# Optimization experiments

Measured on AMD Instinct MI355X. Metric: run time of the kernel, lower is better.

Reference implementation:

```python
import jax, jax.numpy as jnp
import numpy as np

N_NODES = 100000
N_EDGES = 1200000
NODE_DIM = 128
HIDDEN = 64
N_POSTS = 50000


def setup_inputs() -> dict:
    key = jax.random.key(0)
    ks = jax.random.split(key, 10)
    s = 1.0 / np.sqrt(NODE_DIM)
    sh = 1.0 / np.sqrt(HIDDEN)
    return {
        "node_features": jax.random.normal(ks[0], (N_NODES, NODE_DIM), dtype=jnp.float32),
        "edge_index": jax.random.randint(ks[1], (2, N_EDGES), 0, N_NODES, dtype=jnp.int64) if jax.config.jax_enable_x64 else jax.random.randint(ks[1], (2, N_EDGES), 0, N_NODES, dtype=jnp.int32),
        "post_mask": jax.random.randint(ks[2], (N_POSTS,), 0, N_NODES, dtype=jnp.int32),
        "W_enc": jax.random.uniform(ks[3], (NODE_DIM, HIDDEN), jnp.float32, -s, s),
        "b_enc": jax.random.uniform(ks[4], (HIDDEN,), jnp.float32, -s, s),
        "W_conv": jax.random.uniform(ks[5], (HIDDEN, HIDDEN), jnp.float32, -sh, sh),
        "b_conv": jax.random.uniform(ks[6], (HIDDEN,), jnp.float32, -sh, sh),
        "W_out": jax.random.uniform(ks[7], (HIDDEN, 1), jnp.float32, -sh, sh),
        "b_out": jax.random.uniform(ks[8], (1,), jnp.float32, -sh, sh),
    }


def reference(node_features, edge_index, post_mask, W_enc, b_enc, W_conv, b_conv, W_out, b_out):
    # encode: relu(Linear)
    node_emb = jax.nn.relu(node_features @ W_enc + b_enc)  # [N, H]
    src, dst = edge_index[0], edge_index[1]
    # per-edge gather then scatter-add into destination nodes (segment sum)
    messages = jax.ops.segment_sum(node_emb[src], dst, num_segments=node_emb.shape[0])  # [N, H]
    node_emb = jax.nn.relu((node_emb + messages) @ W_conv + b_conv)  # [N, H]
    post_emb = node_emb[post_mask]  # [P, H]
    out = jax.nn.sigmoid((post_emb @ W_out + b_out).squeeze(-1))  # [P]
    return out
```

## Files before the change

kernel.cpp:

```cpp
#include <hip/hip_runtime.h>
#include <hip/hip_bf16.h>
#include <math.h>


#define HIDDEN 64
#define NODE_DIM 128
#define SCAN_CHUNK 1024

typedef __attribute__((ext_vector_type(8))) short short8;
typedef __attribute__((ext_vector_type(4))) float floatx4;

union F2B { short8 s; __hip_bfloat162 h[4]; };

__device__ inline short8 cvt8(const float4& p, const float4& q) {
    F2B u;
    u.h[0] = __float22bfloat162_rn(make_float2(p.x, p.y));
    u.h[1] = __float22bfloat162_rn(make_float2(p.z, p.w));
    u.h[2] = __float22bfloat162_rn(make_float2(q.x, q.y));
    u.h[3] = __float22bfloat162_rn(make_float2(q.z, q.w));
    return u.s;
}

__device__ inline void cvt8_split(const float4& p, const float4& q,
                                  short8& hi, short8& lo) {
    const float f[8] = {p.x, p.y, p.z, p.w, q.x, q.y, q.z, q.w};
    F2B uh, ul;
    #pragma unroll
    for (int jj = 0; jj < 4; ++jj) {
        const float2 v = make_float2(f[2 * jj], f[2 * jj + 1]);
        const __hip_bfloat162 h = __float22bfloat162_rn(v);
        const float2 hv = __bfloat1622float2(h);
        ul.h[jj] = __float22bfloat162_rn(make_float2(v.x - hv.x, v.y - hv.y));
        uh.h[jj] = h;
    }
    hi = uh.s; lo = ul.s;
}

__global__ __launch_bounds__(256) void k_pre(
    const int* __restrict__ post, unsigned int* __restrict__ bits,
    int* __restrict__ nodelist, int* __restrict__ listCnt,
    int* __restrict__ count, int n_posts, int n_nodes)
{
    const int gtid = blockIdx.x * 256 + threadIdx.x;
    if (gtid < n_nodes) count[gtid] = 0;
    if (gtid < n_posts) {
        const int n = post[gtid];
        const unsigned int bit = 1u << (n & 31);
        const unsigned int old = atomicOr(&bits[n >> 5], bit);
        if (!(old & bit)) {
            const int i = atomicAdd(listCnt, 1);
            nodelist[i] = n;
        }
    }
}

__global__ __launch_bounds__(256) void k_encode_count(
    const float* __restrict__ A, const float* __restrict__ We,
    const float* __restrict__ be, __hip_bfloat16* __restrict__ emb16,
    const int* __restrict__ dsts, const unsigned int* __restrict__ bits,
    int* __restrict__ count, int n_nodes, int n_tiles, int n_edges)
{
    const int lane = threadIdx.x & 63;
    const int r    = lane & 15;
    const int quad = lane >> 4;

    short8 Wb[4][4];
    #pragma unroll
    for (int ks = 0; ks < 4; ++ks)
        #pragma unroll
        for (int nt = 0; nt < 4; ++nt) {
            F2B u;
            #pragma unroll
            for (int jj = 0; jj < 4; ++jj) {
                const int k0 = ks * 32 + quad * 8 + 2 * jj;
                const float lo = We[(size_t)k0 * HIDDEN + nt * 16 + r];
                const float hi = We[(size_t)(k0 + 1) * HIDDEN + nt * 16 + r];
                u.h[jj] = __float22bfloat162_rn(make_float2(lo, hi));
            }
            Wb[ks][nt] = u.s;
        }
    float bias[4];
    #pragma unroll
    for (int nt = 0; nt < 4; ++nt) bias[nt] = be[nt * 16 + r];

    const int wid    = (blockIdx.x * 256 + threadIdx.x) >> 6;
    const int nwaves = gridDim.x * 4;
    for (int t = wid; t < n_tiles; t += nwaves) {
        const float* Arow = A + (size_t)t * 16 * NODE_DIM + (size_t)r * NODE_DIM + quad * 8;
        float4 a[4][2];
        #pragma unroll
        for (int ks = 0; ks < 4; ++ks) {
            a[ks][0] = *(const float4*)(Arow + ks * 32);
            a[ks][1] = *(const float4*)(Arow + ks * 32 + 4);
        }
        floatx4 acc[4] = {};
        #pragma unroll
        for (int ks = 0; ks < 4; ++ks) {
            const short8 af = cvt8(a[ks][0], a[ks][1]);
            #pragma unroll
            for (int nt = 0; nt < 4; ++nt)
                acc[nt] = __builtin_amdgcn_mfma_f32_16x16x32_bf16(af, Wb[ks][nt], acc[nt], 0, 0, 0);
        }
        #pragma unroll
        for (int nt = 0; nt < 4; ++nt)
            #pragma unroll
            for (int g = 0; g < 4; ++g) {
                const int node = t * 16 + quad * 4 + g;
                const float h = fmaxf(acc[nt][g] + bias[nt], 0.0f);
                emb16[(size_t)node * HIDDEN + nt * 16 + r] = __float2bfloat16(h);
            }
    }
    const int rem = n_nodes - n_tiles * 16;
    if (rem > 0 && wid == 0) {
        for (int n = n_tiles * 16; n < n_nodes; ++n) {
            float acc = be[lane];
            const float* row = A + (size_t)n * NODE_DIM;
            for (int k = 0; k < NODE_DIM; ++k)
                acc = fmaf(row[k], We[(size_t)k * HIDDEN + lane], acc);
            emb16[(size_t)n * HIDDEN + lane] = __float2bfloat16(fmaxf(acc, 0.0f));
        }
    }

    const int stride = gridDim.x * 256;
    for (int e = blockIdx.x * 256 + threadIdx.x; e < n_edges; e += stride) {
        const int d = dsts[e];
        if ((bits[d >> 5] >> (d & 31)) & 1u) atomicAdd(&count[d], 1);
    }
}

__global__ __launch_bounds__(256) void k_scan_lb(
    const int* __restrict__ count, int* __restrict__ row_start,
    unsigned int* __restrict__ partials, int n)
{
    __shared__ int s[256];
    __shared__ int sExc;
    const int b = blockIdx.x, tid = threadIdx.x;
    const int base = b * SCAN_CHUNK + tid * 4;
    int c0 = (base + 0 < n) ? count[base + 0] : 0;
    int c1 = (base + 1 < n) ? count[base + 1] : 0;
    int c2 = (base + 2 < n) ? count[base + 2] : 0;
    int c3 = (base + 3 < n) ? count[base + 3] : 0;
    const int t = c0 + c1 + c2 + c3;
    s[tid] = t;
    __syncthreads();
    #pragma unroll
    for (int off = 1; off < 256; off <<= 1) {
        int v = (tid >= off) ? s[tid - off] : 0;
        __syncthreads();
        s[tid] += v;
        __syncthreads();
    }
    const int total = s[255];

    if (b == 0) {
        if (tid == 0) {
            __hip_atomic_store(&partials[0], (2u << 30) | (unsigned int)total,
                               __ATOMIC_RELEASE, __HIP_MEMORY_SCOPE_AGENT);
            sExc = 0;
        }
    } else {
        if (tid == 0) {
            __hip_atomic_store(&partials[b], (1u << 30) | (unsigned int)total,
                               __ATOMIC_RELEASE, __HIP_MEMORY_SCOPE_AGENT);
        }
        if (tid < 64) {
            int exc = 0;
            int winEnd = b;
            while (true) {
                const int j = winEnd - 64 + tid;
                const unsigned int v = (j >= 0)
                    ? __hip_atomic_load(&partials[j], __ATOMIC_ACQUIRE,
                                        __HIP_MEMORY_SCOPE_AGENT)
                    : (2u << 30);
                const unsigned int st = v >> 30;
                if (__ballot(st == 0u)) {
                    __builtin_amdgcn_s_sleep(1);
                    continue;
                }
                const unsigned long long b2 = __ballot(st == 2u);
                int contrib;
                bool done;
                if (b2) {
                    const int hi = 63 - __clzll(b2);
                    contrib = (tid >= hi) ? (int)(v & 0x3FFFFFFFu) : 0;
                    done = true;
                } else {
                    contrib = (int)(v & 0x3FFFFFFFu);
                    done = false;
                }
                #pragma unroll
                for (int off = 1; off < 64; off <<= 1)
                    contrib += __shfl_xor(contrib, off);
                exc += contrib;
                if (done) break;
                winEnd -= 64;
            }
            if (tid == 0) {
                __hip_atomic_store(&partials[b],
                                   (2u << 30) | (unsigned int)(exc + total),
                                   __ATOMIC_RELEASE, __HIP_MEMORY_SCOPE_AGENT);
                sExc = exc;
            }
        }
    }
    __syncthreads();
    int run = sExc + s[tid] - t;
    if (base + 0 < n) row_start[base + 0] = run;           run += c0;
    if (base + 1 < n) row_start[base + 1] = run;           run += c1;
    if (base + 2 < n) row_start[base + 2] = run;           run += c2;
    if (base + 3 < n) row_start[base + 3] = run;
}

__global__ __launch_bounds__(256) void k_fill(
    const int* __restrict__ srcs, const int* __restrict__ dsts,
    const unsigned int* __restrict__ bits, int* __restrict__ row_start,
    int* __restrict__ slots, int n_edges)
{
    const int stride = gridDim.x * 256;
    for (int e = blockIdx.x * 256 + threadIdx.x; e < n_edges; e += stride) {
        const int d = dsts[e];
        if (!((bits[d >> 5] >> (d & 31)) & 1u)) continue;
        const int idx = atomicAdd(&row_start[d], 1);
        slots[idx] = srcs[e];
    }
}

__global__ __launch_bounds__(256) void k_gather(
    const int* __restrict__ nodelist, const int* __restrict__ listCnt,
    const int* __restrict__ row_end, const int* __restrict__ count,
    const int* __restrict__ slots, const __hip_bfloat16* __restrict__ emb16,
    float* __restrict__ msg_c)
{
    const int lane = threadIdx.x & 63;
    const int j    = lane & 7;
    const int g    = lane >> 3;
    const int gw   = (blockIdx.x * 256 + threadIdx.x) >> 6;
    const int nw   = gridDim.x * 4;
    const int nc   = listCnt[0];

    for (int i = gw; i < nc; i += nw) {
        const int n    = nodelist[i];
        const int m    = count[n];
        const int base = row_end[n] - m;

        float2 a0 = {0.f, 0.f}, a1 = {0.f, 0.f}, a2 = {0.f, 0.f}, a3 = {0.f, 0.f};
        #define ACC8(v)  do { F2B u; u.s = (v); float2 t;                       \
            t = __bfloat1622float2(u.h[0]); a0.x += t.x; a0.y += t.y;           \
            t = __bfloat1622float2(u.h[1]); a1.x += t.x; a1.y += t.y;           \
            t = __bfloat1622float2(u.h[2]); a2.x += t.x; a2.y += t.y;           \
            t = __bfloat1622float2(u.h[3]); a3.x += t.x; a3.y += t.y; } while (0)

        if (g == 0) {
            const short8 v = *(const short8*)(emb16 + (size_t)n * HIDDEN + j * 8);
            ACC8(v);
        }
        int c = g;
        for (; c + 8 < m; c += 16) {
            const int s0 = slots[base + c];
            const int s1 = slots[base + c + 8];
            const short8 v0 = *(const short8*)(emb16 + (size_t)s0 * HIDDEN + j * 8);
            const short8 v1 = *(const short8*)(emb16 + (size_t)s1 * HIDDEN + j * 8);
            ACC8(v0); ACC8(v1);
        }
        for (; c < m; c += 8) {
            const int s0 = slots[base + c];
            const short8 v0 = *(const short8*)(emb16 + (size_t)s0 * HIDDEN + j * 8);
            ACC8(v0);
        }
        #undef ACC8

        #pragma unroll
        for (int off = 8; off < 64; off <<= 1) {
            a0.x += __shfl_xor(a0.x, off); a0.y += __shfl_xor(a0.y, off);
            a1.x += __shfl_xor(a1.x, off); a1.y += __shfl_xor(a1.y, off);
            a2.x += __shfl_xor(a2.x, off); a2.y += __shfl_xor(a2.y, off);
            a3.x += __shfl_xor(a3.x, off); a3.y += __shfl_xor(a3.y, off);
        }
        if (g == 0) {
            float4* dst = (float4*)(msg_c + (size_t)i * HIDDEN + j * 8);
            dst[0] = make_float4(a0.x, a0.y, a1.x, a1.y);
            dst[1] = make_float4(a2.x, a2.y, a3.x, a3.y);
        }
    }
}

__global__ __launch_bounds__(256) void k_head_mfma(
    const int* __restrict__ listCnt, const int* __restrict__ nodelist,
    const float* __restrict__ msg_c,
    const float* __restrict__ Wc, const float* __restrict__ bc,
    const float* __restrict__ Wo, const float* __restrict__ bo,
    float* __restrict__ res)
{
    const int lane = threadIdx.x & 63;
    const int r    = lane & 15;
    const int quad = lane >> 4;

    short8 Wb[2][4];
    #pragma unroll
    for (int ks = 0; ks < 2; ++ks)
        #pragma unroll
        for (int nt = 0; nt < 4; ++nt) {
            F2B u;
            #pragma unroll
            for (int jj = 0; jj < 4; ++jj) {
                const int k0 = ks * 32 + quad * 8 + 2 * jj;
                const float lo = Wc[(size_t)k0 * HIDDEN + nt * 16 + r];
                const float hi = Wc[(size_t)(k0 + 1) * HIDDEN + nt * 16 + r];
                u.h[jj] = __float22bfloat162_rn(make_float2(lo, hi));
            }
            Wb[ks][nt] = u.s;
        }
    float bias[4], wo[4];
    #pragma unroll
    for (int nt = 0; nt < 4; ++nt) { bias[nt] = bc[nt * 16 + r]; wo[nt] = Wo[nt * 16 + r]; }
    const float bo_s = bo[0];

    const int nc      = listCnt[0];
    const int n_tiles = (nc + 15) / 16;
    const int wid     = (blockIdx.x * 256 + threadIdx.x) >> 6;
    const int nwaves  = gridDim.x * 4;

    for (int tile = wid; tile < n_tiles; tile += nwaves) {
        const int i0  = tile * 16;
        const int row = i0 + r;
        floatx4 acc[4] = {};
        #pragma unroll
        for (int ks = 0; ks < 2; ++ks) {
            float4 f0 = make_float4(0.f, 0.f, 0.f, 0.f), f1 = f0;
            if (row < nc) {
                const float* src = msg_c + (size_t)row * HIDDEN + ks * 32 + quad * 8;
                f0 = *(const float4*)src;
                f1 = *(const float4*)(src + 4);
            }
            short8 ah, al;
            cvt8_split(f0, f1, ah, al);
            #pragma unroll
            for (int nt = 0; nt < 4; ++nt) {
                acc[nt] = __builtin_amdgcn_mfma_f32_16x16x32_bf16(ah, Wb[ks][nt], acc[nt], 0, 0, 0);
                acc[nt] = __builtin_amdgcn_mfma_f32_16x16x32_bf16(al, Wb[ks][nt], acc[nt], 0, 0, 0);
            }
        }
        float r4[4];
        #pragma unroll
        for (int gg = 0; gg < 4; ++gg) {
            float part = 0.0f;
            #pragma unroll
            for (int nt = 0; nt < 4; ++nt)
                part += fmaxf(acc[nt][gg] + bias[nt], 0.0f) * wo[nt];
            part += __shfl_xor(part, 1);
            part += __shfl_xor(part, 2);
            part += __shfl_xor(part, 4);
            part += __shfl_xor(part, 8);
            r4[gg] = part;
        }
        if (r == 0) {
            #pragma unroll
            for (int gg = 0; gg < 4; ++gg) {
                const int idx = i0 + quad * 4 + gg;
                if (idx < nc)
                    res[nodelist[idx]] = 1.0f / (1.0f + __expf(-(r4[gg] + bo_s)));
            }
        }
    }
}

__global__ __launch_bounds__(256) void k_out(
    const int* __restrict__ post, const float* __restrict__ res,
    float* __restrict__ out, int n_posts)
{
    const int p = blockIdx.x * 256 + threadIdx.x;
    if (p < n_posts) out[p] = res[post[p]];
}

extern "C" void kernel_launch(void* const* d_in, const int* in_sizes, int n_in,
                              void* d_out, int out_size, void* d_ws, size_t ws_size,
                              hipStream_t stream) {
    const float* A    = (const float*)d_in[0];
    const int*   ei   = (const int*)  d_in[1];
    const int*   post = (const int*)  d_in[2];
    const float* We   = (const float*)d_in[3];
    const float* be   = (const float*)d_in[4];
    const float* Wc   = (const float*)d_in[5];
    const float* bc   = (const float*)d_in[6];
    const float* Wo   = (const float*)d_in[7];
    const float* bo   = (const float*)d_in[8];
    float* out = (float*)d_out;

    const int n_nodes = in_sizes[0] / NODE_DIM;
    const int n_edges = in_sizes[1] / 2;
    const int n_posts = in_sizes[2];

    char* p = (char*)d_ws;
    __hip_bfloat16* emb16 = (__hip_bfloat16*)p;  p += (size_t)n_nodes * HIDDEN * 2;
    float* msg_c    = (float*)p;              p += (size_t)n_posts * HIDDEN * 4;
    int*   slots    = (int*)p;                p += (size_t)n_edges * 4;
    char* zbase = p;
    unsigned int* bits = (unsigned int*)p;    p += ((size_t)(n_nodes + 31) / 32 + 32) * 4;
    int*   listCnt  = (int*)p;                p += 256;
    unsigned int* partials = (unsigned int*)p; p += 1024;
    const size_t zbytes = (size_t)(p - zbase);
    int*   count    = (int*)p;                p += (size_t)n_nodes * 4;
    int*   row_start= (int*)p;                p += (size_t)n_nodes * 4;
    int*   nodelist = (int*)p;                p += (size_t)n_nodes * 4;
    float* res      = (float*)p;              p += (size_t)n_nodes * 4;

    const int* srcs = ei;
    const int* dsts = ei + n_edges;
    const int nb = (n_nodes + SCAN_CHUNK - 1) / SCAN_CHUNK;
    const int n_tiles = n_nodes / 16;

    hipMemsetAsync(zbase, 0, zbytes, stream);
    k_pre<<<(n_nodes + 255) / 256, 256, 0, stream>>>(post, bits, nodelist, listCnt, count, n_posts, n_nodes);
    k_encode_count<<<(n_tiles + 3) / 4, 256, 0, stream>>>(A, We, be, emb16, dsts, bits, count, n_nodes, n_tiles, n_edges);
    k_scan_lb<<<nb, 256, 0, stream>>>(count, row_start, partials, n_nodes);
    k_fill<<<2048, 256, 0, stream>>>(srcs, dsts, bits, row_start, slots, n_edges);
    k_gather<<<8192, 256, 0, stream>>>(nodelist, listCnt, row_start, count, slots, emb16, msg_c);
    k_head_mfma<<<1024, 256, 0, stream>>>(listCnt, nodelist, msg_c, Wc, bc, Wo, bo, res);
    k_out<<<(n_posts + 255) / 256, 256, 0, stream>>>(post, res, out, n_posts);
}
```

Measured before the change: 202.5 us.

## Stage encoder weights in LDS, prefetch next tile, use persistent grid

The encode kernel now copies the 128x64 encoder weight matrix into shared memory once per block and builds the bf16 MFMA fragments from LDS instead of strided global reads. The launch changes from one block per four tiles to a fixed 512-block persistent grid. Each wave register-double-buffers its input tile, loading the next tile's rows while running MFMAs on the current one. This cuts redundant weight loads across many blocks and hides global load latency, at the cost of 32KB LDS per block and extra registers, which may lower occupancy.

After: 201.3 us. About the same (-0.6%).

```diff
diff --git a/kernel.cpp b/kernel.cpp
--- a/kernel.cpp
+++ b/kernel.cpp
@@ -60,6 +60,17 @@
     const int* __restrict__ dsts, const unsigned int* __restrict__ bits,
     int* __restrict__ count, int n_nodes, int n_tiles, int n_edges)
 {
+    __shared__ float sWe[NODE_DIM * HIDDEN];
+
+    {
+        const float4* src = (const float4*)We;
+        float4* dst = (float4*)sWe;
+        #pragma unroll
+        for (int i = 0; i < (NODE_DIM * HIDDEN / 4) / 256; ++i)
+            dst[i * 256 + threadIdx.x] = src[i * 256 + threadIdx.x];
+    }
+    __syncthreads();
+
     const int lane = threadIdx.x & 63;
     const int r    = lane & 15;
     const int quad = lane >> 4;
@@ -73,8 +84,8 @@
             #pragma unroll
             for (int jj = 0; jj < 4; ++jj) {
                 const int k0 = ks * 32 + quad * 8 + 2 * jj;
-                const float lo = We[(size_t)k0 * HIDDEN + nt * 16 + r];
-                const float hi = We[(size_t)(k0 + 1) * HIDDEN + nt * 16 + r];
+                const float lo = sWe[k0 * HIDDEN + nt * 16 + r];
+                const float hi = sWe[(k0 + 1) * HIDDEN + nt * 16 + r];
                 u.h[jj] = __float22bfloat162_rn(make_float2(lo, hi));
             }
             Wb[ks][nt] = u.s;
@@ -85,13 +96,32 @@
 
     const int wid    = (blockIdx.x * 256 + threadIdx.x) >> 6;
     const int nwaves = gridDim.x * 4;
-    for (int t = wid; t < n_tiles; t += nwaves) {
+
+    int t = wid;
+    float4 a[4][2];
+    if (t < n_tiles) {
         const float* Arow = A + (size_t)t * 16 * NODE_DIM + (size_t)r * NODE_DIM + quad * 8;
-        float4 a[4][2];
         #pragma unroll
         for (int ks = 0; ks < 4; ++ks) {
             a[ks][0] = *(const float4*)(Arow + ks * 32);
             a[ks][1] = *(const float4*)(Arow + ks * 32 + 4);
+        }
+    }
+    while (t < n_tiles) {
+        const int tn = t + nwaves;
+        float4 b[4][2];
+        #pragma unroll
+        for (int ks = 0; ks < 4; ++ks) {
+            b[ks][0] = make_float4(0.f, 0.f, 0.f, 0.f);
+            b[ks][1] = make_float4(0.f, 0.f, 0.f, 0.f);
+        }
+        if (tn < n_tiles) {
+            const float* Brow = A + (size_t)tn * 16 * NODE_DIM + (size_t)r * NODE_DIM + quad * 8;
+            #pragma unroll
+            for (int ks = 0; ks < 4; ++ks) {
+                b[ks][0] = *(const float4*)(Brow + ks * 32);
+                b[ks][1] = *(const float4*)(Brow + ks * 32 + 4);
+            }
         }
         floatx4 acc[4] = {};
         #pragma unroll
@@ -109,6 +139,12 @@
                 const float h = fmaxf(acc[nt][g] + bias[nt], 0.0f);
                 emb16[(size_t)node * HIDDEN + nt * 16 + r] = __float2bfloat16(h);
             }
+        #pragma unroll
+        for (int ks = 0; ks < 4; ++ks) {
+            a[ks][0] = b[ks][0];
+            a[ks][1] = b[ks][1];
+        }
+        t = tn;
     }
     const int rem = n_nodes - n_tiles * 16;
     if (rem > 0 && wid == 0) {
@@ -411,7 +447,7 @@
 
     hipMemsetAsync(zbase, 0, zbytes, stream);
     k_pre<<<(n_nodes + 255) / 256, 256, 0, stream>>>(post, bits, nodelist, listCnt, count, n_posts, n_nodes);
-    k_encode_count<<<(n_tiles + 3) / 4, 256, 0, stream>>>(A, We, be, emb16, dsts, bits, count, n_nodes, n_tiles, n_edges);
+    k_encode_count<<<512, 256, 0, stream>>>(A, We, be, emb16, dsts, bits, count, n_nodes, n_tiles, n_edges);
     k_scan_lb<<<nb, 256, 0, stream>>>(count, row_start, partials, n_nodes);
     k_fill<<<2048, 256, 0, stream>>>(srcs, dsts, bits, row_start, slots, n_edges);
     k_gather<<<8192, 256, 0, stream>>>(nodelist, listCnt, row_start, count, slots, emb16, msg_c);
```
